# Performance work log

Measured on AMD Instinct MI355X. Metric: run time of the kernel, lower is better.

The kernel has to match this reference:

```python
import jax, jax.numpy as jnp
import numpy as np

B, C, H, W = 4, 64, 224, 224
MAX_SEG = 256       # max superpixel label -> segment buffer size 257
MAX_SEG_REF = 256


def _superfeatures(feat, labels, num_seg):
    """scatter_max segment pooling over interior pixels.
    feat [B,C,H,W], labels [B,1,H,W] int -> [B,C,num_seg]."""
    b, c = feat.shape[:2]
    src = feat[:, :, 1:-1, 1:-1].reshape(b, c, -1)   # [B,C,P]
    idx = labels[:, 0, 1:-1, 1:-1].reshape(b, -1)    # [B,P]

    def one(s, i):
        m = jax.ops.segment_max(s.T, i, num_segments=num_seg)  # [S,C]
        return jnp.where(jnp.isneginf(m), 0.0, m).T            # empty segments -> 0

    return jax.vmap(one)(src, idx)                   # [B,C,S]


def _chan_norm(x, eps=1e-5):
    # per-superpixel: subtract channel mean, divide by channel L2 norm (torch dim=1)
    xm = x - jnp.mean(x, axis=1, keepdims=True)
    return xm / (jnp.linalg.norm(xm, axis=1, keepdims=True) + eps)


def setup_inputs():
    key = jax.random.key(0)
    ks = jax.random.split(key, 11)
    rn = lambda k, sh: jax.random.normal(k, sh, dtype=jnp.float32)
    return {
        "feat_target": rn(ks[0], (B, C, H, W)),
        "feat_ref": rn(ks[1], (B, C, H, W)),
        "feat_rgb_ref": rn(ks[2], (B, C, H, W)),
        "Wq": rn(ks[3], (C, C)) * 0.1, "bq": rn(ks[4], (C,)) * 0.1,
        "Wk": rn(ks[5], (C, C)) * 0.1, "bk": rn(ks[6], (C,)) * 0.1,
        "Wv": rn(ks[7], (C, C)) * 0.1, "bv": rn(ks[8], (C,)) * 0.1,
        "label_mask_target": jax.random.randint(ks[9], (B, 1, H, W), 0, MAX_SEG + 1, dtype=jnp.int32),
        "label_mask_ref": jax.random.randint(ks[10], (B, 1, H, W), 0, MAX_SEG_REF + 1, dtype=jnp.int32),
        "max_segments": MAX_SEG,
        "max_segments_ref": MAX_SEG_REF,
    }


def reference(feat_target, feat_ref, feat_rgb_ref, Wq, bq, Wk, bk, Wv, bv,
              label_mask_target, label_mask_ref, max_segments, max_segments_ref):
    S_t = max_segments + 1
    S_r = max_segments_ref + 1
    b, c, h, w = feat_target.shape

    # Superfeatures: segment pooling (scatter_max)
    enc_t = _superfeatures(feat_target, label_mask_target, S_t)   # [B,C,S_t]
    enc_r = _superfeatures(feat_ref, label_mask_ref, S_r)         # [B,C,S_r]
    enc_v = _superfeatures(feat_rgb_ref, label_mask_ref, S_r)     # [B,C,S_r]

    # per-sample variable lengths (label_target / label_ref in the torch loop)
    n_t = jnp.max(label_mask_target.reshape(b, -1), axis=1) + 1
    n_r = jnp.max(label_mask_ref.reshape(b, -1), axis=1) + 1
    tmask = jnp.arange(S_t)[None, :] < n_t[:, None]               # [B,S_t]
    rmask = jnp.arange(S_r)[None, :] < n_r[:, None]               # [B,S_r]

    # Superattention_conv (batched over the original per-sample loop)
    q = jnp.einsum('oc,bcn->bon', Wq, _chan_norm(enc_t)) + bq[None, :, None]
    k = jnp.einsum('oc,bcm->bom', Wk, _chan_norm(enc_r)) + bk[None, :, None]
    v = jnp.einsum('oc,bcm->bom', Wv, enc_v) + bv[None, :, None]  # value conv on raw rgb feats

    sim = jnp.einsum('bcn,bcm->bnm', q, k) / 0.01                 # temperature 0.01
    sim = jnp.where(rmask[:, None, :], sim, -jnp.inf)             # mask invalid ref cols
    attn = jax.nn.softmax(sim, axis=2) * tmask[:, :, None]        # softmax dim=2, zero pad rows

    wg = jnp.einsum('bnm,bcm->bcn', attn, v)                      # [B,C,S_t] (transposed wg_ref)

    # Unpool_features: gather back to pixel grid
    idx = jnp.broadcast_to(label_mask_target.reshape(b, 1, -1), (b, c, h * w))
    unpool = jnp.take_along_axis(wg, idx, axis=2).reshape(b, c, h, w)
    return unpool
```

## Files before the change

kernel.cpp:

```cpp
#include <hip/hip_runtime.h>
#include <math.h>

#define BB 4
#define CC 64
#define HH 224
#define WW 224
#define HWW (HH*WW)
#define SS 257
#define IH 222
#define IW 222
#define NG (222*56)
#define NI ((NG + 511) / 512)

__device__ __forceinline__ unsigned fkey(float f) {
    unsigned u = __float_as_uint(f);
    return (u & 0x80000000u) ? ~u : (u | 0x80000000u);
}
__device__ __forceinline__ float funkey(unsigned k) {
    return (k & 0x80000000u) ? __uint_as_float(k & 0x7FFFFFFFu) : __uint_as_float(~k);
}
#define SENT 0x007FFFFFu

__global__ __launch_bounds__(512) void pool_kernel(
    const float* __restrict__ fT, const float* __restrict__ fR,
    const float* __restrict__ fV,
    const int* __restrict__ labT, const int* __restrict__ labR,
    float* __restrict__ enc, int* __restrict__ nmax)
{
    __shared__ unsigned seg[SS];
    __shared__ int wmax[8];
    const int c = blockIdx.x, b = blockIdx.y, z = blockIdx.z;
    const float* src = (z == 0) ? fT : (z == 1) ? fR : fV;
    const int*   lab = (z == 0) ? labT : labR;
    const bool do_nmax = (c == 0) && (z < 2);

    for (int i = threadIdx.x; i < SS; i += 512) seg[i] = SENT;
    __syncthreads();

    const float4* sp4 = (const float4*)(src + (size_t)(b * CC + c) * HWW);
    const int*    lp  = lab + (size_t)b * HWW;
    const int4*   lp4 = (const int4*)lp;

    int lmax = -1;

    int gi = threadIdx.x;
    bool act = gi < NG;
    float4 v = {}; int4 l = {}; int curg = 0;
    {
        int h = gi / 56; int g = gi - h * 56; curg = g;
        if (act) { int idx4 = (h + 1) * 56 + g; v = sp4[idx4]; l = lp4[idx4]; }
    }
    for (int it = 0; it < NI; ++it) {
        int gin = gi + 512;
        bool actn = gin < NG;
        float4 vn = {}; int4 ln = {}; int gn = 0;
        if (actn) {
            int hn = gin / 56; gn = gin - hn * 56;
            int idx4 = (hn + 1) * 56 + gn;
            vn = sp4[idx4]; ln = lp4[idx4];
        }
        if (act) {
            if (do_nmax)
                lmax = max(lmax, max(max(l.x, l.y), max(l.z, l.w)));
            unsigned kx = fkey(v.x), ky = fkey(v.y), kz = fkey(v.z), kw = fkey(v.w);
            if (curg != 0  && kx > seg[l.x]) atomicMax(&seg[l.x], kx);
            if (ky > seg[l.y]) atomicMax(&seg[l.y], ky);
            if (kz > seg[l.z]) atomicMax(&seg[l.z], kz);
            if (curg != 55 && kw > seg[l.w]) atomicMax(&seg[l.w], kw);
        }
        v = vn; l = ln; act = actn; gi = gin; curg = gn;
    }

    if (do_nmax && threadIdx.x < 448) {
        int t = threadIdx.x;
        int off = (t < 224) ? t : (223 * 224 + (t - 224));
        lmax = max(lmax, lp[off]);
    }
    #pragma unroll
    for (int o = 32; o; o >>= 1) lmax = max(lmax, __shfl_xor(lmax, o, 64));
    if ((threadIdx.x & 63) == 0) wmax[threadIdx.x >> 6] = lmax;
    __syncthreads();

    if (do_nmax && threadIdx.x == 0) {
        int m = wmax[0];
        #pragma unroll
        for (int i = 1; i < 8; ++i) m = max(m, wmax[i]);
        nmax[z * BB + b] = m + 1;
    }

    float* op = enc + (size_t)((z * BB + b) * CC + c) * SS;
    for (int i = threadIdx.x; i < SS; i += 512) {
        unsigned k = seg[i];
        op[i] = (k == SENT) ? 0.0f : funkey(k);
    }
}

__global__ __launch_bounds__(512) void qkv_kernel(
    const float* __restrict__ enc,
    const float* __restrict__ Wq, const float* __restrict__ bq,
    const float* __restrict__ Wk, const float* __restrict__ bk,
    const float* __restrict__ Wv, const float* __restrict__ bv,
    float* __restrict__ qkv)
{
    const int z = blockIdx.z, b = blockIdx.y;
    const int wid = threadIdx.x >> 6, lane = threadIdx.x & 63;
    const int n = blockIdx.x * 8 + wid;
    if (n >= SS) return;

    const float* Wm = (z == 0) ? Wq : (z == 1) ? Wk : Wv;
    const float* bm = (z == 0) ? bq : (z == 1) ? bk : bv;
    const float* ep = enc + (size_t)((z * BB + b) * CC) * SS + n;

    float x = ep[(size_t)lane * SS];
    if (z != 2) {
        float s = x;
        for (int o = 32; o; o >>= 1) s += __shfl_xor(s, o, 64);
        float xm = x - s * (1.0f / 64.0f);
        float s2 = xm * xm;
        for (int o = 32; o; o >>= 1) s2 += __shfl_xor(s2, o, 64);
        x = xm / (sqrtf(s2) + 1e-5f);
    }
    float acc = bm[lane];
    #pragma unroll
    for (int cI = 0; cI < 64; ++cI) {
        float xc = __shfl(x, cI, 64);
        acc = fmaf(Wm[lane * 64 + cI], xc, acc);
    }
    qkv[(size_t)((z * BB + b) * SS + n) * CC + lane] = acc;
}

__global__ __launch_bounds__(256) void attn_kernel(
    const float* __restrict__ qkv, const int* __restrict__ nmax,
    float* __restrict__ wg)
{
    const int n = blockIdx.x, b = blockIdx.y, t = threadIdx.x;
    __shared__ float qs[CC];
    __shared__ float sim[512];
    __shared__ float red[256];
    __shared__ float pv[4][64];

    const int nT = nmax[b], nR = nmax[BB + b];
    float* wp = wg + (size_t)(b * SS + n) * CC;
    if (n >= nT) {
        if (t < CC) wp[t] = 0.0f;
        return;
    }
    const float* q = qkv + (size_t)(0 * BB + b) * SS * CC;
    const float* k = qkv + (size_t)(1 * BB + b) * SS * CC;
    const float* v = qkv + (size_t)(2 * BB + b) * SS * CC;

    if (t < CC) qs[t] = q[(size_t)n * CC + t];
    sim[t] = -INFINITY;
    sim[t + 256] = -INFINITY;
    __syncthreads();

    for (int m = t; m < SS; m += 256) {
        float s = -INFINITY;
        if (m < nR) {
            const float4* kr = (const float4*)(k + (size_t)m * CC);
            float acc = 0.0f;
            #pragma unroll
            for (int i = 0; i < 16; ++i) {
                float4 kv = kr[i];
                acc += qs[4*i+0]*kv.x + qs[4*i+1]*kv.y + qs[4*i+2]*kv.z + qs[4*i+3]*kv.w;
            }
            s = acc * 100.0f;
        }
        sim[m] = s;
    }
    __syncthreads();

    red[t] = fmaxf(sim[t], sim[t + 256]);
    __syncthreads();
    for (int s = 128; s > 0; s >>= 1) {
        if (t < s) red[t] = fmaxf(red[t], red[t + s]);
        __syncthreads();
    }
    const float mx = red[0];
    __syncthreads();

    float psum = 0.0f;
    for (int m = t; m < SS; m += 256) {
        float e = expf(sim[m] - mx);
        sim[m] = e;
        psum += e;
    }
    red[t] = psum;
    __syncthreads();
    for (int s = 128; s > 0; s >>= 1) {
        if (t < s) red[t] += red[t + s];
        __syncthreads();
    }
    const float rdenom = 1.0f / red[0];

    const int g = t >> 6, c = t & 63;
    float acc = 0.0f;
    for (int m = g; m < SS; m += 4)
        acc = fmaf(sim[m], v[(size_t)m * CC + c], acc);
    pv[g][c] = acc;
    __syncthreads();
    if (t < CC)
        wp[t] = (pv[0][t] + pv[1][t] + pv[2][t] + pv[3][t]) * rdenom;
}

__global__ __launch_bounds__(256) void unpool_kernel(
    const float* __restrict__ wg, const int* __restrict__ labT,
    float* __restrict__ out)
{
    const int idx = blockIdx.x * 256 + threadIdx.x;
    if (idx >= BB * HWW) return;
    const int b = idx / HWW, hw = idx - b * HWW;
    const int l = labT[idx];
    const float4* row = (const float4*)(wg + (size_t)(b * SS + l) * CC);
    float* op = out + (size_t)b * CC * HWW + hw;
    #pragma unroll
    for (int i = 0; i < 16; ++i) {
        float4 r = row[i];
        op[(size_t)(4*i+0) * HWW] = r.x;
        op[(size_t)(4*i+1) * HWW] = r.y;
        op[(size_t)(4*i+2) * HWW] = r.z;
        op[(size_t)(4*i+3) * HWW] = r.w;
    }
}

extern "C" void kernel_launch(void* const* d_in, const int* in_sizes, int n_in,
                              void* d_out, int out_size, void* d_ws, size_t ws_size,
                              hipStream_t stream) {
    (void)in_sizes; (void)n_in; (void)out_size; (void)ws_size;
    const float* fT  = (const float*)d_in[0];
    const float* fR  = (const float*)d_in[1];
    const float* fV  = (const float*)d_in[2];
    const float* Wq  = (const float*)d_in[3];
    const float* bq  = (const float*)d_in[4];
    const float* Wk  = (const float*)d_in[5];
    const float* bk  = (const float*)d_in[6];
    const float* Wv  = (const float*)d_in[7];
    const float* bv  = (const float*)d_in[8];
    const int* labT  = (const int*)d_in[9];
    const int* labR  = (const int*)d_in[10];
    float* out = (float*)d_out;

    float* enc  = (float*)d_ws;
    float* qkv  = enc + 3 * BB * CC * SS;
    float* wg   = qkv + 3 * BB * CC * SS;
    int*   nmax = (int*)(wg + BB * CC * SS);

    pool_kernel<<<dim3(CC, BB, 3), 512, 0, stream>>>(fT, fR, fV, labT, labR, enc, nmax);
    qkv_kernel<<<dim3((SS + 7) / 8, BB, 3), 512, 0, stream>>>(enc, Wq, bq, Wk, bk, Wv, bv, qkv);
    attn_kernel<<<dim3(SS, BB), 256, 0, stream>>>(qkv, nmax, wg);
    unpool_kernel<<<(BB * HWW + 255) / 256, 256, 0, stream>>>(wg, labT, out);
}
```

Before: 82.23 us.

## Split segment pooling over row chunks with 8 channels per block and global atomic merge

The pooling kernel now gives each block 8 channels and a chunk of 28 rows, so one label load serves 8 channels. Partial per-block maxima are merged into the workspace with global atomicMax on order-preserving keys. A new init kernel fills the workspace with the sentinel beforehand, and the qkv kernel decodes the keys. This adds an extra launch and global atomic traffic in exchange for more parallel blocks and fewer label reads.

```diff
diff --git a/kernel.cpp b/kernel.cpp
--- a/kernel.cpp
+++ b/kernel.cpp
@@ -7,10 +7,10 @@
 #define WW 224
 #define HWW (HH*WW)
 #define SS 257
-#define IH 222
-#define IW 222
-#define NG (222*56)
-#define NI ((NG + 511) / 512)
+#define CPB 8
+#define NRC 8
+#define RPC 28
+#define ENCW (3*BB*CC*SS)
 
 __device__ __forceinline__ unsigned fkey(float f) {
     unsigned u = __float_as_uint(f);
@@ -21,82 +21,97 @@
 }
 #define SENT 0x007FFFFFu
 
-__global__ __launch_bounds__(512) void pool_kernel(
+__global__ __launch_bounds__(256) void init_kernel(unsigned* __restrict__ enc,
+                                                   int* __restrict__ nmax) {
+    int i = blockIdx.x * 256 + threadIdx.x;
+    if (i < ENCW / 4) ((uint4*)enc)[i] = make_uint4(SENT, SENT, SENT, SENT);
+    if (i < 2 * BB) nmax[i] = 0;
+}
+
+__global__ __launch_bounds__(256) void pool_kernel(
     const float* __restrict__ fT, const float* __restrict__ fR,
     const float* __restrict__ fV,
     const int* __restrict__ labT, const int* __restrict__ labR,
-    float* __restrict__ enc, int* __restrict__ nmax)
-{
-    __shared__ unsigned seg[SS];
-    __shared__ int wmax[8];
-    const int c = blockIdx.x, b = blockIdx.y, z = blockIdx.z;
+    unsigned* __restrict__ enc, int* __restrict__ nmax)
+{
+    __shared__ unsigned seg[CPB * SS];
+    __shared__ int wmax[4];
+    const int cg = blockIdx.x, rc = blockIdx.y;
+    const int z = blockIdx.z >> 2, b = blockIdx.z & 3;
     const float* src = (z == 0) ? fT : (z == 1) ? fR : fV;
     const int*   lab = (z == 0) ? labT : labR;
-    const bool do_nmax = (c == 0) && (z < 2);
-
-    for (int i = threadIdx.x; i < SS; i += 512) seg[i] = SENT;
-    __syncthreads();
-
-    const float4* sp4 = (const float4*)(src + (size_t)(b * CC + c) * HWW);
+
+    for (int i = threadIdx.x; i < CPB * SS; i += 256) seg[i] = SENT;
+    __syncthreads();
+
+    const int h0 = rc * RPC;
+    const int h1 = min(222, h0 + RPC);
+    const int ngroups = (h1 - h0) * 56;
+
     const int*    lp  = lab + (size_t)b * HWW;
     const int4*   lp4 = (const int4*)lp;
-
+    const float4* fp4 = (const float4*)(src + (size_t)(b * CC + cg * CPB) * HWW);
+    const int PS4 = HWW / 4;
+
+    const bool do_nmax = (cg == 0) && (z < 2);
     int lmax = -1;
 
-    int gi = threadIdx.x;
-    bool act = gi < NG;
-    float4 v = {}; int4 l = {}; int curg = 0;
-    {
-        int h = gi / 56; int g = gi - h * 56; curg = g;
-        if (act) { int idx4 = (h + 1) * 56 + g; v = sp4[idx4]; l = lp4[idx4]; }
-    }
-    for (int it = 0; it < NI; ++it) {
-        int gin = gi + 512;
-        bool actn = gin < NG;
-        float4 vn = {}; int4 ln = {}; int gn = 0;
-        if (actn) {
-            int hn = gin / 56; gn = gin - hn * 56;
-            int idx4 = (hn + 1) * 56 + gn;
-            vn = sp4[idx4]; ln = lp4[idx4];
+    for (int gi = threadIdx.x; gi < ngroups; gi += 256) {
+        int h = gi / 56;
+        int g = gi - h * 56;
+        int idx4 = (h0 + h + 1) * 56 + g;
+        int4   l  = lp4[idx4];
+        float4 f0 = fp4[idx4          ];
+        float4 f1 = fp4[idx4 + 1 * PS4];
+        float4 f2 = fp4[idx4 + 2 * PS4];
+        float4 f3 = fp4[idx4 + 3 * PS4];
+        float4 f4 = fp4[idx4 + 4 * PS4];
+        float4 f5 = fp4[idx4 + 5 * PS4];
+        float4 f6 = fp4[idx4 + 6 * PS4];
+        float4 f7 = fp4[idx4 + 7 * PS4];
+        if (do_nmax)
+            lmax = max(lmax, max(max(l.x, l.y), max(l.z, l.w)));
+        const bool mx = (g != 0), mw = (g != 55);
+#define PROC(F, CCN) do { \
+        unsigned kx = fkey(F.x), ky = fkey(F.y), kz = fkey(F.z), kw = fkey(F.w); \
+        unsigned* sg = seg + (CCN) * SS; \
+        if (mx && kx > sg[l.x]) atomicMax(&sg[l.x], kx); \
+        if (ky > sg[l.y]) atomicMax(&sg[l.y], ky); \
+        if (kz > sg[l.z]) atomicMax(&sg[l.z], kz); \
+        if (mw && kw > sg[l.w]) atomicMax(&sg[l.w], kw); } while (0)
+        PROC(f0, 0); PROC(f1, 1); PROC(f2, 2); PROC(f3, 3);
+        PROC(f4, 4); PROC(f5, 5); PROC(f6, 6); PROC(f7, 7);
+#undef PROC
+    }
+
+    if (do_nmax && threadIdx.x < 56) {
+        if (rc == 0) {
+            int4 l = lp4[threadIdx.x];
+            lmax = max(lmax, max(max(l.x, l.y), max(l.z, l.w)));
         }
-        if (act) {
-            if (do_nmax)
-                lmax = max(lmax, max(max(l.x, l.y), max(l.z, l.w)));
-            unsigned kx = fkey(v.x), ky = fkey(v.y), kz = fkey(v.z), kw = fkey(v.w);
-            if (curg != 0  && kx > seg[l.x]) atomicMax(&seg[l.x], kx);
-            if (ky > seg[l.y]) atomicMax(&seg[l.y], ky);
-            if (kz > seg[l.z]) atomicMax(&seg[l.z], kz);
-            if (curg != 55 && kw > seg[l.w]) atomicMax(&seg[l.w], kw);
+        if (rc == NRC - 1) {
+            int4 l = lp4[223 * 56 + threadIdx.x];
+            lmax = max(lmax, max(max(l.x, l.y), max(l.z, l.w)));
         }
-        v = vn; l = ln; act = actn; gi = gin; curg = gn;
-    }
-
-    if (do_nmax && threadIdx.x < 448) {
-        int t = threadIdx.x;
-        int off = (t < 224) ? t : (223 * 224 + (t - 224));
-        lmax = max(lmax, lp[off]);
     }
     #pragma unroll
     for (int o = 32; o; o >>= 1) lmax = max(lmax, __shfl_xor(lmax, o, 64));
     if ((threadIdx.x & 63) == 0) wmax[threadIdx.x >> 6] = lmax;
     __syncthreads();
-
     if (do_nmax && threadIdx.x == 0) {
-        int m = wmax[0];
-        #pragma unroll
-        for (int i = 1; i < 8; ++i) m = max(m, wmax[i]);
-        nmax[z * BB + b] = m + 1;
-    }
-
-    float* op = enc + (size_t)((z * BB + b) * CC + c) * SS;
-    for (int i = threadIdx.x; i < SS; i += 512) {
+        int m = max(max(wmax[0], wmax[1]), max(wmax[2], wmax[3]));
+        atomicMax(&nmax[z * BB + b], m + 1);
+    }
+
+    unsigned* gp = enc + (size_t)((z * BB + b) * CC + cg * CPB) * SS;
+    for (int i = threadIdx.x; i < CPB * SS; i += 256) {
         unsigned k = seg[i];
-        op[i] = (k == SENT) ? 0.0f : funkey(k);
+        if (k != SENT) atomicMax(&gp[i], k);
     }
 }
 
 __global__ __launch_bounds__(512) void qkv_kernel(
-    const float* __restrict__ enc,
+    const unsigned* __restrict__ enc,
     const float* __restrict__ Wq, const float* __restrict__ bq,
     const float* __restrict__ Wk, const float* __restrict__ bk,
     const float* __restrict__ Wv, const float* __restrict__ bv,
@@ -109,9 +124,10 @@
 
     const float* Wm = (z == 0) ? Wq : (z == 1) ? Wk : Wv;
     const float* bm = (z == 0) ? bq : (z == 1) ? bk : bv;
-    const float* ep = enc + (size_t)((z * BB + b) * CC) * SS + n;
-
-    float x = ep[(size_t)lane * SS];
+    const unsigned* ep = enc + (size_t)((z * BB + b) * CC) * SS + n;
+
+    unsigned kraw = ep[(size_t)lane * SS];
+    float x = (kraw == SENT) ? 0.0f : funkey(kraw);
     if (z != 2) {
         float s = x;
         for (int o = 32; o; o >>= 1) s += __shfl_xor(s, o, 64);
@@ -240,12 +256,13 @@
     const int* labR  = (const int*)d_in[10];
     float* out = (float*)d_out;
 
-    float* enc  = (float*)d_ws;
-    float* qkv  = enc + 3 * BB * CC * SS;
+    unsigned* enc = (unsigned*)d_ws;
+    float* qkv  = (float*)d_ws + ENCW;
     float* wg   = qkv + 3 * BB * CC * SS;
     int*   nmax = (int*)(wg + BB * CC * SS);
 
-    pool_kernel<<<dim3(CC, BB, 3), 512, 0, stream>>>(fT, fR, fV, labT, labR, enc, nmax);
+    init_kernel<<<(ENCW / 4 + 255) / 256, 256, 0, stream>>>(enc, nmax);
+    pool_kernel<<<dim3(CPB, NRC, 12), 256, 0, stream>>>(fT, fR, fV, labT, labR, enc, nmax);
     qkv_kernel<<<dim3((SS + 7) / 8, BB, 3), 512, 0, stream>>>(enc, Wq, bq, Wk, bk, Wv, bv, qkv);
     attn_kernel<<<dim3(SS, BB), 256, 0, stream>>>(qkv, nmax, wg);
     unpool_kernel<<<(BB * HWW + 255) / 256, 256, 0, stream>>>(wg, labT, out);
```

New measurement: 91.29 us. +11.0%, slower.
